# Optimization experiments

Hardware: AMD Instinct MI355X
Metric: run time of the kernel (lower is better)

The kernel has to match this reference:

```python
import jax, jax.numpy as jnp
import numpy as np

INPUT_DIM = 1024
GRID_SIZE = 5
SPLINE_ORDER = 3
GRID_MIN, GRID_MAX = -1.5, 1.5
NUM_BASIS = GRID_SIZE + SPLINE_ORDER  # 8
LN_EPS = 1e-5


def _spline_grid():
    # grid = arange(-spline_order, grid_size+spline_order+1)*h + grid_min, per input dim
    h = (GRID_MAX - GRID_MIN) / GRID_SIZE
    g = jnp.arange(-SPLINE_ORDER, GRID_SIZE + SPLINE_ORDER + 1, dtype=jnp.float32) * h + GRID_MIN  # [12]
    return jnp.broadcast_to(g, (INPUT_DIM, g.shape[0]))  # [D, 12]


def _rbf_grid():
    return jnp.linspace(GRID_MIN, GRID_MAX, NUM_BASIS, dtype=jnp.float32)  # [8]


def _b_splines(x):
    # x: [B, D] -> bases [B, D, grid_size+spline_order]
    grid = _spline_grid()  # [D, G]
    xe = x[..., None]  # [B, D, 1]
    bases = ((xe >= grid[:, :-1]) & (xe < grid[:, 1:])).astype(x.dtype)  # [B, D, G-1]
    for k in range(1, SPLINE_ORDER + 1):
        left = (xe - grid[:, :-(k + 1)]) / (grid[:, k:-1] - grid[:, :-(k + 1)])
        right = (grid[:, k + 1:] - xe) / (grid[:, k + 1:] - grid[:, 1:-k])
        bases = left * bases[:, :, :-1] + right * bases[:, :, 1:]
    return bases  # [B, D, NUM_BASIS]


def setup_inputs() -> dict:
    key = jax.random.key(0)
    k1, k2, k3 = jax.random.split(key, 3)
    B, D, O = 8192, INPUT_DIM, 1024
    x = jax.random.normal(k1, (B, D), dtype=jnp.float32)
    ln_weight = jnp.ones((D,), dtype=jnp.float32)
    ln_bias = jnp.zeros((D,), dtype=jnp.float32)
    # kaiming_uniform(a=sqrt(5)) ~ U(-1/sqrt(fan_in), 1/sqrt(fan_in))
    base_weight = jax.random.uniform(k2, (O, D), jnp.float32, -1.0, 1.0) / np.sqrt(D)
    spline_weight = jax.random.uniform(k3, (O, D * NUM_BASIS), jnp.float32, -1.0, 1.0) / np.sqrt(D * NUM_BASIS)
    return {"x": x, "ln_weight": ln_weight, "ln_bias": ln_bias,
            "base_weight": base_weight, "spline_weight": spline_weight}


def reference(x, ln_weight, ln_bias, base_weight, spline_weight):
    B = x.shape[0]
    # LayerNorm
    mu = jnp.mean(x, axis=-1, keepdims=True)
    var = jnp.mean((x - mu) ** 2, axis=-1, keepdims=True)
    xn = (x - mu) * jax.lax.rsqrt(var + LN_EPS) * ln_weight + ln_bias  # [B, D]
    # base branch: SiLU + linear
    base_out = jax.nn.silu(xn) @ base_weight.T  # [B, O]
    # spline branch
    spl = _b_splines(xn).reshape(B, -1)  # [B, D*8]
    spline_out = spl @ spline_weight.T
    # rbf branch (same weight)
    denom = (GRID_MAX - GRID_MIN) / (NUM_BASIS - 1)
    rbf = jnp.exp(-(((xn[..., None] - _rbf_grid()) / denom) ** 2)).reshape(B, -1)  # [B, D*8]
    rbf_out = rbf @ spline_weight.T
    return base_out + rbf_out + spline_out
```

## Files before the change

kernel.cpp:

```cpp
#include <hip/hip_runtime.h>

#define B_ROWS 8192
#define D_IN   1024
#define NOUT   1024
#define KB     1024
#define KS     8192
#define GM     256
#define GN     128
#define GK     64
#define GKS    128

#define TBL_N  2048
#define TBL_X0 (-5.5f)
#define TBL_W  11.0f

typedef __attribute__((ext_vector_type(4))) float f32x4;
typedef __attribute__((ext_vector_type(4))) int   i32x4;
typedef __attribute__((ext_vector_type(8))) short bf16x8;

#define SCALE_F 63.5f
#define SCALE_W 11494.728f

__device__ __forceinline__ unsigned short f2bf(float f) {
  union { float f; unsigned u; } v; v.f = f;
  unsigned r = v.u + 0x7fffu + ((v.u >> 16) & 1u);
  return (unsigned short)(r >> 16);
}

__device__ __forceinline__ unsigned pk4(float a, float b, float c, float d, float s) {
  int qa = (int)rintf(fminf(fmaxf(a * s, -127.f), 127.f));
  int qb = (int)rintf(fminf(fmaxf(b * s, -127.f), 127.f));
  int qc = (int)rintf(fminf(fmaxf(c * s, -127.f), 127.f));
  int qd = (int)rintf(fminf(fmaxf(d * s, -127.f), 127.f));
  return (unsigned)(qa & 255) | ((unsigned)(qb & 255) << 8) |
         ((unsigned)(qc & 255) << 16) | ((unsigned)(qd & 255) << 24);
}

__device__ __forceinline__ void load_lds16(const void* g, void* l) {
  __builtin_amdgcn_global_load_lds(
      (const __attribute__((address_space(1))) unsigned int*)g,
      (__attribute__((address_space(3))) unsigned int*)l, 16, 0, 0);
}

__device__ __forceinline__ void barrier_raw() {
  asm volatile("" ::: "memory");
  __builtin_amdgcn_s_barrier();
  asm volatile("" ::: "memory");
}

__global__ __launch_bounds__(256) void tbl_kernel(unsigned char* __restrict__ T) {
  const int k = blockIdx.x * 256 + threadIdx.x;
  const float xn = TBL_X0 + (TBL_W / TBL_N) * k;
  float b[11];
#pragma unroll
  for (int j = 0; j < 11; ++j) {
    const float gj = 0.6f * j - 3.3f;
    b[j] = (xn >= gj && xn < gj + 0.6f) ? 1.f : 0.f;
  }
#pragma unroll
  for (int kk = 1; kk <= 3; ++kk) {
    const float inv = 1.f / (0.6f * kk);
#pragma unroll
    for (int j = 0; j <= 10 - kk; ++j) {
      const float gj = 0.6f * j - 3.3f;
      b[j] = (xn - gj) * inv * b[j] + (gj + 0.6f * (kk + 1) - xn) * inv * b[j + 1];
    }
  }
  float f[8];
#pragma unroll
  for (int j = 0; j < 8; ++j) {
    const float c = -1.5f + (3.f / 7.f) * j;
    const float tt = (xn - c) * (7.f / 3.f);
    f[j] = b[j] + __expf(-tt * tt);
  }
  *reinterpret_cast<uint2*>(T + (size_t)k * 8) =
      make_uint2(pk4(f[0], f[1], f[2], f[3], SCALE_F),
                 pk4(f[4], f[5], f[6], f[7], SCALE_F));
}

__global__ __launch_bounds__(256) void wconv_b(
    const float* __restrict__ bw, unsigned short* __restrict__ Wb) {
  const size_t idx = ((size_t)blockIdx.x * 256 + threadIdx.x) * 4;
  float4 f = *reinterpret_cast<const float4*>(bw + idx);
  union { unsigned short us[4]; uint2 u2; } o;
  o.us[0] = f2bf(f.x); o.us[1] = f2bf(f.y); o.us[2] = f2bf(f.z); o.us[3] = f2bf(f.w);
  *reinterpret_cast<uint2*>(Wb + idx) = o.u2;
}

__global__ __launch_bounds__(256) void wconv_s(
    const float* __restrict__ sw, unsigned char* __restrict__ Ws) {
  const size_t base = ((size_t)blockIdx.x * 256 + threadIdx.x) * 8;
  float4 v0 = *reinterpret_cast<const float4*>(sw + base);
  float4 v1 = *reinterpret_cast<const float4*>(sw + base + 4);
  *reinterpret_cast<uint2*>(Ws + base) =
      make_uint2(pk4(v0.x, v0.y, v0.z, v0.w, SCALE_W),
                 pk4(v1.x, v1.y, v1.z, v1.w, SCALE_W));
}

__global__ __launch_bounds__(256) void feat_kernel(
    const float* __restrict__ x, const float* __restrict__ lnw,
    const float* __restrict__ lnb, const unsigned char* __restrict__ T,
    unsigned short* __restrict__ Fb, unsigned char* __restrict__ Fs, int row0) {
  const int row = row0 + blockIdx.x;
  const float* xr = x + (size_t)row * D_IN;
  const int t = threadIdx.x;
  float v[4];
  float s = 0.f, s2 = 0.f;
#pragma unroll
  for (int i = 0; i < 4; ++i) {
    v[i] = xr[t + 256 * i];
    s += v[i];
    s2 += v[i] * v[i];
  }
#pragma unroll
  for (int off = 32; off > 0; off >>= 1) {
    s += __shfl_xor(s, off);
    s2 += __shfl_xor(s2, off);
  }
  __shared__ float red[8];
  const int wid = t >> 6;
  if ((t & 63) == 0) { red[wid] = s; red[4 + wid] = s2; }
  __syncthreads();
  s  = red[0] + red[1] + red[2] + red[3];
  s2 = red[4] + red[5] + red[6] + red[7];
  const float mu = s * (1.f / D_IN);
  const float var = s2 * (1.f / D_IN) - mu * mu;
  const float rstd = rsqrtf(var + 1e-5f);
  unsigned short* fbr = Fb + (size_t)blockIdx.x * KB;
  unsigned char*  fsr = Fs + (size_t)blockIdx.x * KS;
#pragma unroll
  for (int i = 0; i < 4; ++i) {
    const int d = t + 256 * i;
    const float xn = (v[i] - mu) * rstd * lnw[d] + lnb[d];
    const float e = __expf(-xn);
    fbr[d] = f2bf(xn * __builtin_amdgcn_rcpf(1.f + e));
    int ti = (int)rintf((xn - TBL_X0) * (TBL_N / TBL_W));
    ti = min(max(ti, 0), TBL_N - 1);
    *reinterpret_cast<uint2*>(fsr + d * 8) =
        *reinterpret_cast<const uint2*>(T + (size_t)ti * 8);
  }
}

__global__ __launch_bounds__(512, 2) void gemm_fused(
    const unsigned char* __restrict__ Fs, const unsigned char* __restrict__ Ws,
    const unsigned short* __restrict__ Fb, const unsigned short* __restrict__ Wb,
    float* __restrict__ C, int row0) {
  __shared__ __align__(16) char smem[3 * 32768 + 3 * 16384];
  unsigned char* As8 = (unsigned char*)smem;
  unsigned char* Bs8 = (unsigned char*)(smem + 98304);
  const int t = threadIdx.x;
  const int w = t >> 6, l = t & 63;
  const int wr = w >> 1, wc = w & 1;
  const int id = blockIdx.x;
  const int nbm = gridDim.x >> 3;
  int bm, bn;
  if ((nbm & 7) == 0) {
    const int c = id & 7, j = id >> 3, q = nbm >> 3;
    bm = c + 8 * (j % q);
    bn = j / q;
  } else { bm = id % nbm; bn = id / nbm; }

  const int hi = l >> 4, l15 = l & 15, rs = l & 7;
  const int arow = l >> 3;
  const int achk = (l & 7) ^ arow;

  i32x4 acc[4][4] = {};
  {
    const size_t Ab = (size_t)bm * GM * KS;
    const size_t Bb = (size_t)bn * GN * KS;
    auto stageA = [&](int buf, int k0) {
#pragma unroll
      for (int i = 0; i < 4; ++i) {
        const int ch = i * 512 + t;
        const int r = ch >> 3, c = ch & 7;
        load_lds16(Fs + Ab + (size_t)r * KS + k0 + ((c ^ (r & 7)) * 16),
                   As8 + buf * 32768 + ch * 16);
      }
    };
    auto stageB = [&](int buf, int k0) {
#pragma unroll
      for (int i = 0; i < 2; ++i) {
        const int ch = i * 512 + t;
        const int r = ch >> 3, c = ch & 7;
        load_lds16(Ws + Bb + (size_t)r * KS + k0 + ((c ^ (r & 7)) * 16),
                   Bs8 + buf * 16384 + ch * 16);
      }
    };
    const int c0 = (hi ^ rs) * 16;
    const int c1 = ((4 + hi) ^ rs) * 16;
    i32x4 a0[4], a1[4], b0[4], b1[4];
    auto dsread = [&](int buf) {
      const char* Asb = (const char*)(As8 + buf * 32768);
      const char* Bsb = (const char*)(Bs8 + buf * 16384);
#pragma unroll
      for (int m = 0; m < 4; ++m) {
        a0[m] = *reinterpret_cast<const i32x4*>(Asb + (wr * 64 + l15 + m * 16) * 128 + c0);
        a1[m] = *reinterpret_cast<const i32x4*>(Asb + (wr * 64 + l15 + m * 16) * 128 + c1);
      }
#pragma unroll
      for (int n = 0; n < 4; ++n) {
        b0[n] = *reinterpret_cast<const i32x4*>(Bsb + (wc * 64 + l15 + n * 16) * 128 + c0);
        b1[n] = *reinterpret_cast<const i32x4*>(Bsb + (wc * 64 + l15 + n * 16) * 128 + c1);
      }
    };
    auto domfma = [&]() {
      __builtin_amdgcn_s_setprio(1);
#pragma unroll
      for (int m = 0; m < 4; ++m)
#pragma unroll
        for (int n = 0; n < 4; ++n)
          acc[m][n] = __builtin_amdgcn_mfma_i32_16x16x64_i8(a0[m], b0[n], acc[m][n], 0, 0, 0);
#pragma unroll
      for (int m = 0; m < 4; ++m)
#pragma unroll
        for (int n = 0; n < 4; ++n)
          acc[m][n] = __builtin_amdgcn_mfma_i32_16x16x64_i8(a1[m], b1[n], acc[m][n], 0, 0, 0);
      __builtin_amdgcn_s_setprio(0);
    };
    const int NT = KS / GKS;
    stageA(0, 0); stageB(0, 0);
    stageA(1, GKS); stageB(1, GKS);
    asm volatile("s_waitcnt vmcnt(6)" ::: "memory");
    barrier_raw();
    int cur = 0;
    for (int tt = 0; tt < NT; ++tt) {
      int pre = cur + 2; if (pre >= 3) pre -= 3;
      const bool have2 = (tt + 2 < NT);
      dsread(cur);
      if (have2) { stageA(pre, (tt + 2) * GKS); stageB(pre, (tt + 2) * GKS); }
      __builtin_amdgcn_sched_barrier(0);
      domfma();
      if (tt + 1 < NT) {
        if (have2) asm volatile("s_waitcnt vmcnt(6)" ::: "memory");
        else       asm volatile("s_waitcnt vmcnt(0)" ::: "memory");
        barrier_raw();
      }
      cur = cur + 1; if (cur >= 3) cur = 0;
    }
  }
  barrier_raw();

  f32x4 accf[4][4] = {};
  {
    unsigned short* As = (unsigned short*)As8;
    unsigned short* Bs = (unsigned short*)Bs8;
    const size_t Abase = (size_t)bm * GM * KB;
    const size_t Bbase = (size_t)bn * GN * KB;
    auto stageA = [&](int buf, int k0) {
#pragma unroll
      for (int i = 0; i < 4; ++i) {
        const int seg = w * 4 + i;
        load_lds16(Fb + Abase + (size_t)(seg * 8 + arow) * KB + k0 + achk * 8,
                   (char*)(As + buf * 16384) + seg * 1024);
      }
    };
    auto stageB = [&](int buf, int k0) {
#pragma unroll
      for (int i = 0; i < 2; ++i) {
        const int seg = w * 2 + i;
        load_lds16(Wb + Bbase + (size_t)(seg * 8 + arow) * KB + k0 + achk * 8,
                   (char*)(Bs + buf * 8192) + seg * 1024);
      }
    };
    const int rA = wr * 64 + l15;
    const int rB = wc * 64 + l15;
    auto dsread = [&](int buf, int kk, bf16x8* a, bf16x8* b) {
      const int cb = ((kk * 4 + hi) ^ rs) * 16;
#pragma unroll
      for (int m = 0; m < 4; ++m)
        a[m] = *reinterpret_cast<const bf16x8*>(
            (const char*)(As + buf * 16384) + (rA + m * 16) * 128 + cb);
#pragma unroll
      for (int n = 0; n < 4; ++n)
        b[n] = *reinterpret_cast<const bf16x8*>(
            (const char*)(Bs + buf * 8192) + (rB + n * 16) * 128 + cb);
    };
    auto domfma = [&](bf16x8* a, bf16x8* b) {
      __builtin_amdgcn_s_setprio(1);
#pragma unroll
      for (int m = 0; m < 4; ++m)
#pragma unroll
        for (int n = 0; n < 4; ++n)
          accf[m][n] = __builtin_amdgcn_mfma_f32_16x16x32_bf16(a[m], b[n], accf[m][n], 0, 0, 0);
      __builtin_amdgcn_s_setprio(0);
    };
    const int NT = KB / GK;
    stageA(0, 0); stageB(0, 0);
    stageA(1, GK); stageB(1, GK);
    asm volatile("s_waitcnt vmcnt(6)" ::: "memory");
    barrier_raw();
    int cur = 0;
    for (int tt = 0; tt < NT; ++tt) {
      int pre = cur + 2; if (pre >= 3) pre -= 3;
      const bool have2 = (tt + 2 < NT);
      bf16x8 a0[4], b0[4], a1[4], b1[4];
      dsread(cur, 0, a0, b0);
      dsread(cur, 1, a1, b1);
      if (have2) { stageA(pre, (tt + 2) * GK); stageB(pre, (tt + 2) * GK); }
      __builtin_amdgcn_sched_barrier(0);
      domfma(a0, b0);
      __builtin_amdgcn_sched_barrier(0);
      domfma(a1, b1);
      if (tt + 1 < NT) {
        if (have2) asm volatile("s_waitcnt vmcnt(6)" ::: "memory");
        else       asm volatile("s_waitcnt vmcnt(0)" ::: "memory");
        barrier_raw();
      }
      cur = cur + 1; if (cur >= 3) cur = 0;
    }
  }

  const float sc = 1.0f / (SCALE_F * SCALE_W);
  const int crow0 = row0 + bm * GM + wr * 64 + hi * 4;
  const int ccol0 = bn * GN + wc * 64 + l15;
#pragma unroll
  for (int m = 0; m < 4; ++m)
#pragma unroll
    for (int n = 0; n < 4; ++n) {
      float* cp = C + (size_t)(crow0 + m * 16) * NOUT + ccol0 + n * 16;
#pragma unroll
      for (int r = 0; r < 4; ++r)
        cp[(size_t)r * NOUT] = accf[m][n][r] + (float)acc[m][n][r] * sc;
    }
}

extern "C" void kernel_launch(void* const* d_in, const int* in_sizes, int n_in,
                              void* d_out, int out_size, void* d_ws, size_t ws_size,
                              hipStream_t stream) {
  const float* x   = (const float*)d_in[0];
  const float* lnw = (const float*)d_in[1];
  const float* lnb = (const float*)d_in[2];
  const float* bw  = (const float*)d_in[3];
  const float* sw  = (const float*)d_in[4];
  float* out = (float*)d_out;
  char* ws = (char*)d_ws;

  const size_t tbl_bytes = (size_t)TBL_N * 8;
  const size_t wb_bytes = (size_t)NOUT * KB * 2;
  const size_t wsq_bytes = (size_t)NOUT * KS;
  unsigned char*  T   = (unsigned char*)ws;
  unsigned short* Wb  = (unsigned short*)(ws + tbl_bytes);
  unsigned char*  Wsp = (unsigned char*)(ws + tbl_bytes + wb_bytes);
  char* fbase = ws + tbl_bytes + wb_bytes + wsq_bytes;

  const size_t hdr = tbl_bytes + wb_bytes + wsq_bytes;
  const size_t per_row = (size_t)KB * 2 + KS;
  size_t avail = (ws_size > hdr) ? ws_size - hdr : 0;
  long long cm = (long long)(avail / per_row);
  cm &= ~255LL;
  if (cm < 256) cm = 256;
  if (cm > B_ROWS) cm = B_ROWS;
  const int chunkM = (int)cm;
  unsigned short* Fb = (unsigned short*)fbase;
  unsigned char*  Fs = (unsigned char*)(fbase + (size_t)chunkM * KB * 2);

  tbl_kernel<<<TBL_N / 256, 256, 0, stream>>>(T);
  wconv_b<<<(NOUT * KB / 4) / 256, 256, 0, stream>>>(bw, Wb);
  wconv_s<<<(NOUT * KS / 8) / 256, 256, 0, stream>>>(sw, Wsp);
  for (int r0 = 0; r0 < B_ROWS; r0 += chunkM) {
    int rows = B_ROWS - r0; if (rows > chunkM) rows = chunkM;
    feat_kernel<<<rows, 256, 0, stream>>>(x, lnw, lnb, T, Fb, Fs, r0);
    gemm_fused<<<dim3((rows / GM) * (NOUT / GN)), 512, 0, stream>>>(
        Fs, Wsp, Fb, Wb, out, r0);
  }
}
```

Before: 112.7 us.

## Shrink fused GEMM tile to 128x128 with 256 threads and double buffering

Replaces the 256x128 block tile with 512 threads and triple-buffered LDS by a 128x128 tile with 256 threads (4 waves of 64x64) and a double-buffered pipeline that waits on vmcnt(0) at the top of every iteration. LDS drops from 144 KB to 64 KB per block, so more blocks can be resident and the grid doubles. In exchange each block reuses loaded data less (more global/L2 traffic per FLOP), and the shallower prefetch with a full wait each step exposes more memory latency.

```diff
diff --git a/kernel.cpp b/kernel.cpp
--- a/kernel.cpp
+++ b/kernel.cpp
@@ -5,8 +5,7 @@
 #define NOUT   1024
 #define KB     1024
 #define KS     8192
-#define GM     256
-#define GN     128
+#define GT     128
 #define GK     64
 #define GKS    128
 
@@ -141,13 +140,13 @@
   }
 }
 
-__global__ __launch_bounds__(512, 2) void gemm_fused(
+__global__ __launch_bounds__(256, 2) void gemm_fused(
     const unsigned char* __restrict__ Fs, const unsigned char* __restrict__ Ws,
     const unsigned short* __restrict__ Fb, const unsigned short* __restrict__ Wb,
     float* __restrict__ C, int row0) {
-  __shared__ __align__(16) char smem[3 * 32768 + 3 * 16384];
+  __shared__ __align__(16) char smem[65536];
   unsigned char* As8 = (unsigned char*)smem;
-  unsigned char* Bs8 = (unsigned char*)(smem + 98304);
+  unsigned char* Bs8 = (unsigned char*)(smem + 32768);
   const int t = threadIdx.x;
   const int w = t >> 6, l = t & 63;
   const int wr = w >> 1, wc = w & 1;
@@ -161,26 +160,22 @@
   } else { bm = id % nbm; bn = id / nbm; }
 
   const int hi = l >> 4, l15 = l & 15, rs = l & 7;
-  const int arow = l >> 3;
-  const int achk = (l & 7) ^ arow;
 
   i32x4 acc[4][4] = {};
   {
-    const size_t Ab = (size_t)bm * GM * KS;
-    const size_t Bb = (size_t)bn * GN * KS;
-    auto stageA = [&](int buf, int k0) {
+    const size_t Ab = (size_t)bm * GT * KS;
+    const size_t Bb = (size_t)bn * GT * KS;
+    auto stage = [&](int buf, int k0) {
 #pragma unroll
       for (int i = 0; i < 4; ++i) {
-        const int ch = i * 512 + t;
+        const int ch = i * 256 + t;
         const int r = ch >> 3, c = ch & 7;
         load_lds16(Fs + Ab + (size_t)r * KS + k0 + ((c ^ (r & 7)) * 16),
-                   As8 + buf * 32768 + ch * 16);
-      }
-    };
-    auto stageB = [&](int buf, int k0) {
-#pragma unroll
-      for (int i = 0; i < 2; ++i) {
-        const int ch = i * 512 + t;
+                   As8 + buf * 16384 + ch * 16);
+      }
+#pragma unroll
+      for (int i = 0; i < 4; ++i) {
+        const int ch = i * 256 + t;
         const int r = ch >> 3, c = ch & 7;
         load_lds16(Ws + Bb + (size_t)r * KS + k0 + ((c ^ (r & 7)) * 16),
                    Bs8 + buf * 16384 + ch * 16);
@@ -190,7 +185,7 @@
     const int c1 = ((4 + hi) ^ rs) * 16;
     i32x4 a0[4], a1[4], b0[4], b1[4];
     auto dsread = [&](int buf) {
-      const char* Asb = (const char*)(As8 + buf * 32768);
+      const char* Asb = (const char*)(As8 + buf * 16384);
       const char* Bsb = (const char*)(Bs8 + buf * 16384);
 #pragma unroll
       for (int m = 0; m < 4; ++m) {
@@ -218,101 +213,88 @@
       __builtin_amdgcn_s_setprio(0);
     };
     const int NT = KS / GKS;
-    stageA(0, 0); stageB(0, 0);
-    stageA(1, GKS); stageB(1, GKS);
-    asm volatile("s_waitcnt vmcnt(6)" ::: "memory");
-    barrier_raw();
+    stage(0, 0);
     int cur = 0;
     for (int tt = 0; tt < NT; ++tt) {
-      int pre = cur + 2; if (pre >= 3) pre -= 3;
-      const bool have2 = (tt + 2 < NT);
+      asm volatile("s_waitcnt vmcnt(0)" ::: "memory");
+      barrier_raw();
+      if (tt + 1 < NT) stage(cur ^ 1, (tt + 1) * GKS);
       dsread(cur);
-      if (have2) { stageA(pre, (tt + 2) * GKS); stageB(pre, (tt + 2) * GKS); }
       __builtin_amdgcn_sched_barrier(0);
       domfma();
-      if (tt + 1 < NT) {
-        if (have2) asm volatile("s_waitcnt vmcnt(6)" ::: "memory");
-        else       asm volatile("s_waitcnt vmcnt(0)" ::: "memory");
-        barrier_raw();
-      }
-      cur = cur + 1; if (cur >= 3) cur = 0;
+      cur ^= 1;
     }
   }
   barrier_raw();
 
   f32x4 accf[4][4] = {};
   {
-    unsigned short* As = (unsigned short*)As8;
-    unsigned short* Bs = (unsigned short*)Bs8;
-    const size_t Abase = (size_t)bm * GM * KB;
-    const size_t Bbase = (size_t)bn * GN * KB;
-    auto stageA = [&](int buf, int k0) {
+    const size_t Abase = (size_t)bm * GT * KB;
+    const size_t Bbase = (size_t)bn * GT * KB;
+    auto stage = [&](int buf, int k0) {
 #pragma unroll
       for (int i = 0; i < 4; ++i) {
-        const int seg = w * 4 + i;
-        load_lds16(Fb + Abase + (size_t)(seg * 8 + arow) * KB + k0 + achk * 8,
-                   (char*)(As + buf * 16384) + seg * 1024);
-      }
-    };
-    auto stageB = [&](int buf, int k0) {
-#pragma unroll
-      for (int i = 0; i < 2; ++i) {
-        const int seg = w * 2 + i;
-        load_lds16(Wb + Bbase + (size_t)(seg * 8 + arow) * KB + k0 + achk * 8,
-                   (char*)(Bs + buf * 8192) + seg * 1024);
-      }
-    };
-    const int rA = wr * 64 + l15;
-    const int rB = wc * 64 + l15;
-    auto dsread = [&](int buf, int kk, bf16x8* a, bf16x8* b) {
-      const int cb = ((kk * 4 + hi) ^ rs) * 16;
+        const int ch = i * 256 + t;
+        const int r = ch >> 3, c = ch & 7;
+        load_lds16(Fb + Abase + (size_t)r * KB + k0 + ((c ^ (r & 7)) * 8),
+                   As8 + buf * 16384 + ch * 16);
+      }
+#pragma unroll
+      for (int i = 0; i < 4; ++i) {
+        const int ch = i * 256 + t;
+        const int r = ch >> 3, c = ch & 7;
+        load_lds16(Wb + Bbase + (size_t)r * KB + k0 + ((c ^ (r & 7)) * 8),
+                   Bs8 + buf * 16384 + ch * 16);
+      }
+    };
+    bf16x8 a0[4], b0[4], a1[4], b1[4];
+    auto dsread = [&](int buf) {
+      const char* Asb = (const char*)(As8 + buf * 16384);
+      const char* Bsb = (const char*)(Bs8 + buf * 16384);
+      const int cb0 = (hi ^ rs) * 16;
+      const int cb1 = ((4 + hi) ^ rs) * 16;
+#pragma unroll
+      for (int m = 0; m < 4; ++m) {
+        a0[m] = *reinterpret_cast<const bf16x8*>(Asb + (wr * 64 + l15 + m * 16) * 128 + cb0);
+        a1[m] = *reinterpret_cast<const bf16x8*>(Asb + (wr * 64 + l15 + m * 16) * 128 + cb1);
+      }
+#pragma unroll
+      for (int n = 0; n < 4; ++n) {
+        b0[n] = *reinterpret_cast<const bf16x8*>(Bsb + (wc * 64 + l15 + n * 16) * 128 + cb0);
+        b1[n] = *reinterpret_cast<const bf16x8*>(Bsb + (wc * 64 + l15 + n * 16) * 128 + cb1);
+      }
+    };
+    auto domfma = [&]() {
+      __builtin_amdgcn_s_setprio(1);
 #pragma unroll
       for (int m = 0; m < 4; ++m)
-        a[m] = *reinterpret_cast<const bf16x8*>(
-            (const char*)(As + buf * 16384) + (rA + m * 16) * 128 + cb);
-#pragma unroll
-      for (int n = 0; n < 4; ++n)
-        b[n] = *reinterpret_cast<const bf16x8*>(
-            (const char*)(Bs + buf * 8192) + (rB + n * 16) * 128 + cb);
-    };
-    auto domfma = [&](bf16x8* a, bf16x8* b) {
-      __builtin_amdgcn_s_setprio(1);
+#pragma unroll
+        for (int n = 0; n < 4; ++n)
+          accf[m][n] = __builtin_amdgcn_mfma_f32_16x16x32_bf16(a0[m], b0[n], accf[m][n], 0, 0, 0);
 #pragma unroll
       for (int m = 0; m < 4; ++m)
 #pragma unroll
         for (int n = 0; n < 4; ++n)
-          accf[m][n] = __builtin_amdgcn_mfma_f32_16x16x32_bf16(a[m], b[n], accf[m][n], 0, 0, 0);
+          accf[m][n] = __builtin_amdgcn_mfma_f32_16x16x32_bf16(a1[m], b1[n], accf[m][n], 0, 0, 0);
       __builtin_amdgcn_s_setprio(0);
     };
     const int NT = KB / GK;
-    stageA(0, 0); stageB(0, 0);
-    stageA(1, GK); stageB(1, GK);
-    asm volatile("s_waitcnt vmcnt(6)" ::: "memory");
-    barrier_raw();
+    stage(0, 0);
     int cur = 0;
     for (int tt = 0; tt < NT; ++tt) {
-      int pre = cur + 2; if (pre >= 3) pre -= 3;
-      const bool have2 = (tt + 2 < NT);
-      bf16x8 a0[4], b0[4], a1[4], b1[4];
-      dsread(cur, 0, a0, b0);
-      dsread(cur, 1, a1, b1);
-      if (have2) { stageA(pre, (tt + 2) * GK); stageB(pre, (tt + 2) * GK); }
+      asm volatile("s_waitcnt vmcnt(0)" ::: "memory");
+      barrier_raw();
+      if (tt + 1 < NT) stage(cur ^ 1, (tt + 1) * GK);
+      dsread(cur);
       __builtin_amdgcn_sched_barrier(0);
-      domfma(a0, b0);
-      __builtin_amdgcn_sched_barrier(0);
-      domfma(a1, b1);
-      if (tt + 1 < NT) {
-        if (have2) asm volatile("s_waitcnt vmcnt(6)" ::: "memory");
-        else       asm volatile("s_waitcnt vmcnt(0)" ::: "memory");
-        barrier_raw();
-      }
-      cur = cur + 1; if (cur >= 3) cur = 0;
+      domfma();
+      cur ^= 1;
     }
   }
 
   const float sc = 1.0f / (SCALE_F * SCALE_W);
-  const int crow0 = row0 + bm * GM + wr * 64 + hi * 4;
-  const int ccol0 = bn * GN + wc * 64 + l15;
+  const int crow0 = row0 + bm * GT + wr * 64 + hi * 4;
+  const int ccol0 = bn * GT + wc * 64 + l15;
 #pragma unroll
   for (int m = 0; m < 4; ++m)
 #pragma unroll
@@ -360,7 +342,7 @@
   for (int r0 = 0; r0 < B_ROWS; r0 += chunkM) {
     int rows = B_ROWS - r0; if (rows > chunkM) rows = chunkM;
     feat_kernel<<<rows, 256, 0, stream>>>(x, lnw, lnb, T, Fb, Fs, r0);
-    gemm_fused<<<dim3((rows / GM) * (NOUT / GN)), 512, 0, stream>>>(
+    gemm_fused<<<dim3((rows / GT) * (NOUT / GT)), 256, 0, stream>>>(
         Fs, Wsp, Fb, Wb, out, r0);
   }
 }
```

Measured after the change: 111.2 us, median of 3. Within noise of the previous version (-1.4%).
